# Kernel optimization log

Hardware: AMD Instinct MI355X
Metric: run time of the kernel (lower is better)

The kernel has to match this reference:

```python
import jax, jax.numpy as jnp
import numpy as np

B, T = 8, 5
C2, C1, C0 = 128, 256, 512  # in_channels = [C2, C1, C0]


def _ln(x, g, b):
    # LayerNorm over last (channel) axis
    m = jnp.mean(x, axis=-1, keepdims=True)
    v = jnp.var(x, axis=-1, keepdims=True)
    return (x - m) * jax.lax.rsqrt(v + 1e-5) * g + b


def _fuse_branch(x, gc, bc, gr, br, Wcur, Wref, bf, convw, bns, bnb):
    # x: [B, C, T, H, W]
    xt = jnp.transpose(x, (0, 2, 3, 4, 1))            # [B, T, H, W, C] (channel-last, like the permutes)
    cur = xt[:, -1]                                    # [B, H, W, C] last frame
    refs = xt[:, :-1]                                  # [B, T-1, H, W, C]
    # ShiftVSS stand-in: cross-frame fuse with residual (vectorized over T-1 frames)
    cur_proj = jnp.einsum('bhwc,cd->bhwd', _ln(cur, gc, bc), Wcur)        # [B,H,W,C]
    ref_proj = jnp.einsum('bthwc,cd->bthwd', _ln(refs, gr, br), Wref)     # [B,T-1,H,W,C]
    h = cur[:, None] + jax.nn.silu(cur_proj[:, None] + ref_proj + bf)     # [B,T-1,H,W,C]
    # BaseConv 1x1: pointwise conv + folded-BN + SiLU
    y = jax.nn.silu(jnp.einsum('bthwc,cd->bthwd', h, convw) * bns + bnb)  # [B,T-1,H,W,C]
    # fused temporal max + avg pooling (AdaptiveMax/AvgPool3d to T=1)
    pooled = jnp.max(y, axis=1) + jnp.mean(y, axis=1)                     # [B,H,W,C]
    return jnp.transpose(pooled, (0, 3, 1, 2))                            # [B,C,H,W]


def setup_inputs() -> dict:
    key = jax.random.key(0)
    ks = jax.random.split(key, 32)

    def n(k, shape, s=1.0):
        return jax.random.normal(k, shape, dtype=jnp.float32) * s

    d = {}
    d['x2'] = n(ks[0], (B, C2, T, 64, 64))
    d['x1'] = n(ks[1], (B, C1, T, 32, 32))
    d['x0'] = n(ks[2], (B, C0, T, 16, 16))  # unused by forward, kept for signature fidelity
    for i, (p, C) in enumerate([('2', C2), ('1', C1)]):
        o = 3 + i * 4
        d[f'g{p}c'] = jnp.ones((C,), jnp.float32)
        d[f'b{p}c'] = jnp.zeros((C,), jnp.float32)
        d[f'g{p}r'] = jnp.ones((C,), jnp.float32)
        d[f'b{p}r'] = jnp.zeros((C,), jnp.float32)
        d[f'W{p}cur'] = n(ks[o], (C, C), 0.02)
        d[f'W{p}ref'] = n(ks[o + 1], (C, C), 0.02)
        d[f'bias{p}'] = jnp.zeros((C,), jnp.float32)
        d[f'convw{p}'] = n(ks[o + 2], (C, C), 0.02)
        d[f'bns{p}'] = jnp.ones((C,), jnp.float32)
        d[f'bnb{p}'] = jnp.zeros((C,), jnp.float32)
    return d


def reference(x2, x1, x0,
              g2c, b2c, g2r, b2r, W2cur, W2ref, bias2, convw2, bns2, bnb2,
              g1c, b1c, g1r, b1r, W1cur, W1ref, bias1, convw1, bns1, bnb1):
    x2_out = _fuse_branch(x2, g2c, b2c, g2r, b2r, W2cur, W2ref, bias2, convw2, bns2, bnb2)
    x1_out = _fuse_branch(x1, g1c, b1c, g1r, b1r, W1cur, W1ref, bias1, convw1, bns1, bnb1)
    return (x2_out, x1_out)
```

## Files before the change

### kernel.cpp

```cpp
#include <hip/hip_runtime.h>
#include <stdint.h>

#define DI __device__ __forceinline__

typedef __attribute__((ext_vector_type(8))) short short8;
typedef __attribute__((ext_vector_type(4))) short short4v;
typedef __attribute__((ext_vector_type(4))) float f32x4;

DI float bf2f(unsigned short u){ union{unsigned int i; float f;} v; v.i = ((unsigned int)u)<<16; return v.f; }
DI unsigned short f2bf(float f){ union{float f; unsigned int i;} v; v.f=f; return (unsigned short)((v.i + 0x7fffu + ((v.i>>16)&1u))>>16); }
DI float siluf(float x){ return x/(1.f + __expf(-x)); }
DI f32x4 vzero(){ f32x4 z; z[0]=0.f;z[1]=0.f;z[2]=0.f;z[3]=0.f; return z; }
DI f32x4 vsplat(float x){ f32x4 z; z[0]=x;z[1]=x;z[2]=x;z[3]=x; return z; }

struct PrepArgs {
  const float* W[6];
  const float* g[6];
  unsigned short* Wt[6];
  int C[6];
};

__global__ __launch_bounds__(256) void prep_transpose(PrepArgs a){
  int m = blockIdx.z;
  int C = a.C[m];
  int nt = C >> 5;
  if ((int)blockIdx.x >= nt || (int)blockIdx.y >= nt) return;
  __shared__ float tile[32][33];
  int col = threadIdx.x & 31;
  int rr  = threadIdx.x >> 5;
  const float* W = a.W[m];
  const float* g = a.g[m];
  #pragma unroll
  for (int p=0;p<4;++p){
    int r = rr + p*8;
    int cK = blockIdx.x*32 + r;
    int dN = blockIdx.y*32 + col;
    float v = W[(size_t)cK*C + dN];
    if (g) v *= g[cK];
    tile[r][col] = v;
  }
  __syncthreads();
  unsigned short* Wt = a.Wt[m];
  #pragma unroll
  for (int p=0;p<4;++p){
    int r = rr + p*8;
    int dN = blockIdx.y*32 + r;
    int cK = blockIdx.x*32 + col;
    Wt[(size_t)dN*C + cK] = f2bf(tile[col][r]);
  }
}

struct ColArgs {
  const float* W[4]; const float* g[4]; const float* b[4]; const float* extra[4];
  float* ocs[4]; float* obs[4]; int C[4];
};

__global__ __launch_bounds__(256) void prep_colsum(ColArgs a){
  int j = blockIdx.y;
  int C = a.C[j];
  int d0 = blockIdx.x * 64;
  if (d0 >= C) return;
  int dl = threadIdx.x & 63;
  int g  = threadIdx.x >> 6;
  int d  = d0 + dl;
  const float* W = a.W[j]; const float* gv = a.g[j]; const float* bv = a.b[j];
  float cs = 0.f, bs = 0.f;
  for (int c = g; c < C; c += 4){
    float gc = gv[c], bc = bv[c];
    float w = W[(size_t)c*C + d];
    cs += gc*w;
    bs += bc*w;
  }
  __shared__ float rcs[4][64], rbs[4][64];
  rcs[g][dl] = cs; rbs[g][dl] = bs;
  __syncthreads();
  if (threadIdx.x < 64){
    float c0 = rcs[0][dl]+rcs[1][dl]+rcs[2][dl]+rcs[3][dl];
    float b0 = rbs[0][dl]+rbs[1][dl]+rbs[2][dl]+rbs[3][dl];
    if (a.extra[j]) b0 += a.extra[j][d];
    a.ocs[j][d] = c0;
    a.obs[j][d] = b0;
  }
}


template<int C>
DI short8 readFrag(const short* S, int rowBase, int ks, int lane){
  int row = rowBase + (lane & 15);
  int chunk = (ks*4 + ((lane>>4)&3)) ^ (lane & 7);
  return *(const short8*)((const char*)S + row*(2*C) + chunk*16);
}

template<int C>
DI void stageA_x(const float* __restrict__ xb, int strideC, short* As,
                 float* red, float* smean, float* srstd){
  int tid = threadIdx.x;
  int px = tid & 63, g = tid >> 6;
  float sum = 0.f, sq = 0.f;
  #pragma unroll
  for (int it=0; it<C/16; ++it){
    int cb = it*16 + g*4;
    float v0 = xb[(size_t)(cb+0)*strideC + px];
    float v1 = xb[(size_t)(cb+1)*strideC + px];
    float v2 = xb[(size_t)(cb+2)*strideC + px];
    float v3 = xb[(size_t)(cb+3)*strideC + px];
    sum += v0+v1+v2+v3;
    sq  += v0*v0+v1*v1+v2*v2+v3*v3;
    short4v pk;
    pk[0]=(short)f2bf(v0); pk[1]=(short)f2bf(v1); pk[2]=(short)f2bf(v2); pk[3]=(short)f2bf(v3);
    int chunk = cb >> 3;
    *(short4v*)((char*)As + px*(2*C) + ((chunk ^ (px&7))*16) + (cb&7)*2) = pk;
  }
  red[g*64 + px] = sum;
  red[256 + g*64 + px] = sq;
  __syncthreads();
  if (tid < 64){
    float s=0.f, q=0.f;
    #pragma unroll
    for (int gg=0; gg<4; ++gg){ s += red[gg*64+tid]; q += red[256+gg*64+tid]; }
    float m = s*(1.f/C);
    float var = fmaxf(q*(1.f/C) - m*m, 0.f);
    smean[tid] = m;
    srstd[tid] = rsqrtf(var + 1e-5f);
  }
  __syncthreads();
}

template<int C, int ROWS>
DI void stageCopy(const unsigned short* __restrict__ src, short* dst){
  int tid = threadIdx.x;
  constexpr int CH = C/8;
  constexpr int IT = (ROWS*CH)/256;
  #pragma unroll
  for (int it=0; it<IT; ++it){
    int i = tid + it*256;
    int row = i / CH, ch = i % CH;
    short8 v = *(const short8*)(src + (size_t)row*C + ch*8);
    *(short8*)((char*)dst + row*(2*C) + ((ch ^ (row&7))*16)) = v;
  }
}

template<int C>
DI void mfmaLoop(const short* As, const short* Bs, f32x4 acc[2][4], int lane, int wr, int wc){
  #pragma unroll
  for (int ks=0; ks<C/32; ++ks){
    short8 a0 = readFrag<C>(As, wr*32 +  0, ks, lane);
    short8 a1 = readFrag<C>(As, wr*32 + 16, ks, lane);
    short8 b0 = readFrag<C>(Bs, wc*64 +  0, ks, lane);
    short8 b1 = readFrag<C>(Bs, wc*64 + 16, ks, lane);
    short8 b2 = readFrag<C>(Bs, wc*64 + 32, ks, lane);
    short8 b3 = readFrag<C>(Bs, wc*64 + 48, ks, lane);
    acc[0][0] = __builtin_amdgcn_mfma_f32_16x16x32_bf16(a0,b0,acc[0][0],0,0,0);
    acc[0][1] = __builtin_amdgcn_mfma_f32_16x16x32_bf16(a0,b1,acc[0][1],0,0,0);
    acc[0][2] = __builtin_amdgcn_mfma_f32_16x16x32_bf16(a0,b2,acc[0][2],0,0,0);
    acc[0][3] = __builtin_amdgcn_mfma_f32_16x16x32_bf16(a0,b3,acc[0][3],0,0,0);
    acc[1][0] = __builtin_amdgcn_mfma_f32_16x16x32_bf16(a1,b0,acc[1][0],0,0,0);
    acc[1][1] = __builtin_amdgcn_mfma_f32_16x16x32_bf16(a1,b1,acc[1][1],0,0,0);
    acc[1][2] = __builtin_amdgcn_mfma_f32_16x16x32_bf16(a1,b2,acc[1][2],0,0,0);
    acc[1][3] = __builtin_amdgcn_mfma_f32_16x16x32_bf16(a1,b3,acc[1][3],0,0,0);
  }
}

template<int C>
__global__ __launch_bounds__(256) void k1_curproj(
    const float* __restrict__ x, const unsigned short* __restrict__ Wt,
    const float* __restrict__ colsum, const float* __restrict__ bias,
    unsigned short* __restrict__ Pout, unsigned short* __restrict__ curT,
    int Npix, int HW){
  constexpr int T = 5;
  __shared__ __align__(16) short As[64*C];
  __shared__ __align__(16) short Bs[128*C];
  __shared__ float red[512];
  __shared__ float smean[64], srstd[64];

  int n0 = blockIdx.y*128;
  int px0 = blockIdx.x*64;
  int b = px0 / HW, hw0 = px0 % HW;
  const float* xb = x + ((size_t)b*C*T + (T-1))*HW + hw0;

  stageCopy<C,128>(Wt + (size_t)n0*C, Bs);
  stageA_x<C>(xb, T*HW, As, red, smean, srstd);

  int tid = threadIdx.x, lane = tid&63, wid = tid>>6, wr = wid>>1, wc = wid&1, hi = lane>>4;
  f32x4 acc[2][4];
  #pragma unroll
  for (int i=0;i<2;++i)
    #pragma unroll
    for (int j=0;j<4;++j) acc[i][j] = vzero();
  mfmaLoop<C>(As, Bs, acc, lane, wr, wc);

  if (n0 == 0){
    constexpr int CH = C/8;
    #pragma unroll
    for (int it=0; it<(64*CH)/256; ++it){
      int i = tid + it*256;
      int row = i/CH, ch = i%CH;
      short8 v = *(const short8*)((const char*)As + row*(2*C) + ((ch ^ (row&7))*16));
      *(short8*)(curT + (size_t)(px0+row)*C + ch*8) = v;
    }
  }

  #pragma unroll
  for (int nf=0; nf<4; ++nf){
    int d = n0 + wc*64 + nf*16 + (lane&15);
    float cs = colsum[d], bi = bias[d];
    #pragma unroll
    for (int mf=0; mf<2; ++mf){
      #pragma unroll
      for (int r=0; r<4; ++r){
        int pl = wr*32 + mf*16 + hi*4 + r;
        float P = srstd[pl]*(acc[mf][nf][r] - smean[pl]*cs) + bi;
        Pout[(size_t)(px0+pl)*C + d] = f2bf(P);
      }
    }
  }
}

template<int C>
__global__ __launch_bounds__(256) void k2_refproj(
    const float* __restrict__ x, const unsigned short* __restrict__ Wt,
    const float* __restrict__ colsum, const float* __restrict__ biasRf,
    const unsigned short* __restrict__ Pcur, const unsigned short* __restrict__ curT,
    unsigned short* __restrict__ hout, int Npix, int HW){
  constexpr int T = 5;
  __shared__ __align__(16) short As[64*C];
  __shared__ __align__(16) short Bs[128*C];
  __shared__ float red[512];
  __shared__ float smean[64], srstd[64];

  int n0 = blockIdx.y*128;
  int px0 = blockIdx.x*64;
  int t = blockIdx.z;
  int b = px0 / HW, hw0 = px0 % HW;
  const float* xb = x + ((size_t)b*C*T + t)*HW + hw0;

  stageCopy<C,128>(Wt + (size_t)n0*C, Bs);
  stageA_x<C>(xb, T*HW, As, red, smean, srstd);

  int tid = threadIdx.x, lane = tid&63, wid = tid>>6, wr = wid>>1, wc = wid&1, hi = lane>>4;
  f32x4 acc[2][4];
  #pragma unroll
  for (int i=0;i<2;++i)
    #pragma unroll
    for (int j=0;j<4;++j) acc[i][j] = vzero();
  mfmaLoop<C>(As, Bs, acc, lane, wr, wc);

  #pragma unroll
  for (int nf=0; nf<4; ++nf){
    int d = n0 + wc*64 + nf*16 + (lane&15);
    float cs = colsum[d], bi = biasRf[d];
    #pragma unroll
    for (int mf=0; mf<2; ++mf){
      #pragma unroll
      for (int r=0; r<4; ++r){
        int pl = wr*32 + mf*16 + hi*4 + r;
        size_t idx = (size_t)(px0+pl)*C + d;
        float pre = srstd[pl]*(acc[mf][nf][r] - smean[pl]*cs) + bi + bf2f(Pcur[idx]);
        float h = bf2f(curT[idx]) + siluf(pre);
        hout[(size_t)t*Npix*C + idx] = f2bf(h);
      }
    }
  }
}

template<int C>
__global__ __launch_bounds__(256) void k3_conv(
    const unsigned short* __restrict__ h, const unsigned short* __restrict__ WtV,
    const float* __restrict__ bns, const float* __restrict__ bnb,
    float* __restrict__ out, int Npix, int HW){
  constexpr int PB = 133;
  constexpr int AsBytes = 64*C*2;
  constexpr int PoolBytes = 64*PB*4;
  constexpr int U = (AsBytes > PoolBytes) ? AsBytes : PoolBytes;
  __shared__ __align__(16) char uni[U];
  __shared__ __align__(16) short Bs[128*C];
  short* As = (short*)uni;
  float* pool = (float*)uni;

  int n0 = blockIdx.y*128;
  int px0 = blockIdx.x*64;
  int b = px0 / HW, hw0 = px0 % HW;
  int tid = threadIdx.x, lane = tid&63, wid = tid>>6, wr = wid>>1, wc = wid&1, hi = lane>>4;

  stageCopy<C,128>(WtV + (size_t)n0*C, Bs);

  f32x4 mx[2][4], sm[2][4];
  #pragma unroll
  for (int i=0;i<2;++i)
    #pragma unroll
    for (int j=0;j<4;++j){ mx[i][j] = vsplat(-3.0e38f); sm[i][j] = vzero(); }

  for (int t=0; t<4; ++t){
    __syncthreads();
    stageCopy<C,64>(h + ((size_t)t*Npix + px0)*C, As);
    __syncthreads();
    f32x4 acc[2][4];
    #pragma unroll
    for (int i=0;i<2;++i)
      #pragma unroll
      for (int j=0;j<4;++j) acc[i][j] = vzero();
    mfmaLoop<C>(As, Bs, acc, lane, wr, wc);
    #pragma unroll
    for (int nf=0; nf<4; ++nf){
      int d = n0 + wc*64 + nf*16 + (lane&15);
      float s_ = bns[d], b_ = bnb[d];
      #pragma unroll
      for (int mf=0; mf<2; ++mf){
        #pragma unroll
        for (int r=0; r<4; ++r){
          float y = siluf(acc[mf][nf][r]*s_ + b_);
          mx[mf][nf][r] = fmaxf(mx[mf][nf][r], y);
          sm[mf][nf][r] += y;
        }
      }
    }
  }

  __syncthreads();
  #pragma unroll
  for (int nf=0; nf<4; ++nf){
    int dl = wc*64 + nf*16 + (lane&15);
    #pragma unroll
    for (int mf=0; mf<2; ++mf){
      #pragma unroll
      for (int r=0; r<4; ++r){
        int pl = wr*32 + mf*16 + hi*4 + r;
        pool[pl*PB + dl] = mx[mf][nf][r] + 0.25f*sm[mf][nf][r];
      }
    }
  }
  __syncthreads();

  #pragma unroll
  for (int it=0; it<8; ++it){
    int i = tid + it*256;
    int dl = i >> 4;
    int pq = (i & 15) * 4;
    f32x4 vv;
    #pragma unroll
    for (int k=0;k<4;++k) vv[k] = pool[(pq+k)*PB + dl];
    *(f32x4*)(out + (size_t)(b*C + n0 + dl)*HW + hw0 + pq) = vv;
  }
}

extern "C" void kernel_launch(void* const* d_in, const int* in_sizes, int n_in,
                              void* d_out, int out_size, void* d_ws, size_t ws_size,
                              hipStream_t stream) {
  (void)in_sizes; (void)n_in; (void)out_size; (void)ws_size;
  const float* x2    = (const float*)d_in[0];
  const float* x1    = (const float*)d_in[1];
  const float* g2c   = (const float*)d_in[3];
  const float* b2c   = (const float*)d_in[4];
  const float* g2r   = (const float*)d_in[5];
  const float* b2r   = (const float*)d_in[6];
  const float* W2cur = (const float*)d_in[7];
  const float* W2ref = (const float*)d_in[8];
  const float* bias2 = (const float*)d_in[9];
  const float* convw2= (const float*)d_in[10];
  const float* bns2  = (const float*)d_in[11];
  const float* bnb2  = (const float*)d_in[12];
  const float* g1c   = (const float*)d_in[13];
  const float* b1c   = (const float*)d_in[14];
  const float* g1r   = (const float*)d_in[15];
  const float* b1r   = (const float*)d_in[16];
  const float* W1cur = (const float*)d_in[17];
  const float* W1ref = (const float*)d_in[18];
  const float* bias1 = (const float*)d_in[19];
  const float* convw1= (const float*)d_in[20];
  const float* bns1  = (const float*)d_in[21];
  const float* bnb1  = (const float*)d_in[22];

  const int C2 = 128, C1 = 256;
  const int NP2 = 8*64*64, NP1 = 8*32*32;
  const int HW2 = 4096, HW1 = 1024;

  char* ws = (char*)d_ws;
  size_t off = 0;
  auto alloc = [&](size_t bytes){ size_t o = off; off = (off + bytes + 255) & ~(size_t)255; return o; };
  size_t oWtC2 = alloc((size_t)C2*C2*2), oWtR2 = alloc((size_t)C2*C2*2), oWtV2 = alloc((size_t)C2*C2*2);
  size_t oWtC1 = alloc((size_t)C1*C1*2), oWtR1 = alloc((size_t)C1*C1*2), oWtV1 = alloc((size_t)C1*C1*2);
  size_t oColC2 = alloc(C2*4), oBiasC2 = alloc(C2*4), oColR2 = alloc(C2*4), oBiasR2 = alloc(C2*4);
  size_t oColC1 = alloc(C1*4), oBiasC1 = alloc(C1*4), oColR1 = alloc(C1*4), oBiasR1 = alloc(C1*4);
  size_t oP2  = alloc((size_t)NP2*C2*2);
  size_t oCT2 = alloc((size_t)NP2*C2*2);
  size_t oH2  = alloc((size_t)4*NP2*C2*2);
  size_t oP1  = alloc((size_t)NP1*C1*2);
  size_t oCT1 = alloc((size_t)NP1*C1*2);
  size_t oH1  = alloc((size_t)4*NP1*C1*2);

  unsigned short* WtC2 = (unsigned short*)(ws + oWtC2);
  unsigned short* WtR2 = (unsigned short*)(ws + oWtR2);
  unsigned short* WtV2 = (unsigned short*)(ws + oWtV2);
  unsigned short* WtC1 = (unsigned short*)(ws + oWtC1);
  unsigned short* WtR1 = (unsigned short*)(ws + oWtR1);
  unsigned short* WtV1 = (unsigned short*)(ws + oWtV1);
  float* ColC2 = (float*)(ws + oColC2); float* BiasC2 = (float*)(ws + oBiasC2);
  float* ColR2 = (float*)(ws + oColR2); float* BiasR2 = (float*)(ws + oBiasR2);
  float* ColC1 = (float*)(ws + oColC1); float* BiasC1 = (float*)(ws + oBiasC1);
  float* ColR1 = (float*)(ws + oColR1); float* BiasR1 = (float*)(ws + oBiasR1);
  unsigned short* P2  = (unsigned short*)(ws + oP2);
  unsigned short* CT2 = (unsigned short*)(ws + oCT2);
  unsigned short* H2  = (unsigned short*)(ws + oH2);
  unsigned short* P1  = (unsigned short*)(ws + oP1);
  unsigned short* CT1 = (unsigned short*)(ws + oCT1);
  unsigned short* H1  = (unsigned short*)(ws + oH1);

  PrepArgs pa;
  pa.W[0]=W2cur;  pa.g[0]=g2c;     pa.Wt[0]=WtC2; pa.C[0]=C2;
  pa.W[1]=W2ref;  pa.g[1]=g2r;     pa.Wt[1]=WtR2; pa.C[1]=C2;
  pa.W[2]=convw2; pa.g[2]=nullptr; pa.Wt[2]=WtV2; pa.C[2]=C2;
  pa.W[3]=W1cur;  pa.g[3]=g1c;     pa.Wt[3]=WtC1; pa.C[3]=C1;
  pa.W[4]=W1ref;  pa.g[4]=g1r;     pa.Wt[4]=WtR1; pa.C[4]=C1;
  pa.W[5]=convw1; pa.g[5]=nullptr; pa.Wt[5]=WtV1; pa.C[5]=C1;
  prep_transpose<<<dim3(8,8,6), 256, 0, stream>>>(pa);

  ColArgs ca;
  ca.W[0]=W2cur; ca.g[0]=g2c; ca.b[0]=b2c; ca.extra[0]=nullptr; ca.ocs[0]=ColC2; ca.obs[0]=BiasC2; ca.C[0]=C2;
  ca.W[1]=W2ref; ca.g[1]=g2r; ca.b[1]=b2r; ca.extra[1]=bias2;   ca.ocs[1]=ColR2; ca.obs[1]=BiasR2; ca.C[1]=C2;
  ca.W[2]=W1cur; ca.g[2]=g1c; ca.b[2]=b1c; ca.extra[2]=nullptr; ca.ocs[2]=ColC1; ca.obs[2]=BiasC1; ca.C[2]=C1;
  ca.W[3]=W1ref; ca.g[3]=g1r; ca.b[3]=b1r; ca.extra[3]=bias1;   ca.ocs[3]=ColR1; ca.obs[3]=BiasR1; ca.C[3]=C1;
  prep_colsum<<<dim3(4, 4), 256, 0, stream>>>(ca);

  float* out2 = (float*)d_out;
  float* out1 = out2 + (size_t)8*C2*HW2;

  k1_curproj<128><<<dim3(NP2/64, 1),    256, 0, stream>>>(x2, WtC2, ColC2, BiasC2, P2, CT2, NP2, HW2);
  k1_curproj<256><<<dim3(NP1/64, 2),    256, 0, stream>>>(x1, WtC1, ColC1, BiasC1, P1, CT1, NP1, HW1);
  k2_refproj<128><<<dim3(NP2/64, 1, 4), 256, 0, stream>>>(x2, WtR2, ColR2, BiasR2, P2, CT2, H2, NP2, HW2);
  k2_refproj<256><<<dim3(NP1/64, 2, 4), 256, 0, stream>>>(x1, WtR1, ColR1, BiasR1, P1, CT1, H1, NP1, HW1);
  k3_conv<128><<<dim3(NP2/64, 1),       256, 0, stream>>>(H2, WtV2, bns2, bnb2, out2, NP2, HW2);
  k3_conv<256><<<dim3(NP1/64, 2),       256, 0, stream>>>(H1, WtV1, bns1, bnb1, out1, NP1, HW1);
}
```

Measured before the change: 141.1 us.

## Vectorize LN input loads and store cur projections in fragment-native layout

stageA_x now reads x with 16-byte vector loads along the pixel axis and scatters bf16 values into LDS. The LayerNorm statistics are then computed from LDS in a second pass. k1 writes the current-frame projection and the current-frame values in an MFMA-fragment-ordered layout, so k2 can read them with coalesced 16-byte loads instead of scalar strided gathers. k2 stages its h output through LDS so it can write coalesced short8 rows. The cost is an extra barrier and scalar 2-byte LDS scatter stores. The stats are now taken from bf16-rounded values, which slightly changes numerics.

```diff
diff --git a/kernel.cpp b/kernel.cpp
--- a/kernel.cpp
+++ b/kernel.cpp
@@ -4,7 +4,6 @@
 #define DI __device__ __forceinline__
 
 typedef __attribute__((ext_vector_type(8))) short short8;
-typedef __attribute__((ext_vector_type(4))) short short4v;
 typedef __attribute__((ext_vector_type(4))) float f32x4;
 
 DI float bf2f(unsigned short u){ union{unsigned int i; float f;} v; v.i = ((unsigned int)u)<<16; return v.f; }
@@ -95,24 +94,33 @@
 DI void stageA_x(const float* __restrict__ xb, int strideC, short* As,
                  float* red, float* smean, float* srstd){
   int tid = threadIdx.x;
-  int px = tid & 63, g = tid >> 6;
-  float sum = 0.f, sq = 0.f;
-  #pragma unroll
-  for (int it=0; it<C/16; ++it){
-    int cb = it*16 + g*4;
-    float v0 = xb[(size_t)(cb+0)*strideC + px];
-    float v1 = xb[(size_t)(cb+1)*strideC + px];
-    float v2 = xb[(size_t)(cb+2)*strideC + px];
-    float v3 = xb[(size_t)(cb+3)*strideC + px];
-    sum += v0+v1+v2+v3;
-    sq  += v0*v0+v1*v1+v2*v2+v3*v3;
-    short4v pk;
-    pk[0]=(short)f2bf(v0); pk[1]=(short)f2bf(v1); pk[2]=(short)f2bf(v2); pk[3]=(short)f2bf(v3);
-    int chunk = cb >> 3;
-    *(short4v*)((char*)As + px*(2*C) + ((chunk ^ (px&7))*16) + (cb&7)*2) = pk;
-  }
-  red[g*64 + px] = sum;
-  red[256 + g*64 + px] = sq;
+  int lane = tid & 63, w = tid >> 6;
+  #pragma unroll
+  for (int i=0; i<C/16; ++i){
+    int ic = i >> 2, ip = i & 3;
+    int c  = w*(C/4) + ic*16 + (lane & 15);
+    int pq = ip*4 + (lane >> 4);
+    f32x4 v = *(const f32x4*)(xb + (size_t)c*strideC + pq*4);
+    #pragma unroll
+    for (int j=0;j<4;++j){
+      int px = pq*4 + j;
+      *(unsigned short*)((char*)As + px*(2*C) + (((c>>3) ^ (px&7))*16) + (c&7)*2) = f2bf(v[j]);
+    }
+  }
+  __syncthreads();
+  {
+    int px = tid & 63, g = tid >> 6;
+    constexpr int PER = (C/8)/4;
+    float s=0.f, q=0.f;
+    #pragma unroll
+    for (int k=0;k<PER;++k){
+      int ch = g*PER + k;
+      short8 v = *(const short8*)((const char*)As + px*(2*C) + ((ch ^ (px&7))*16));
+      #pragma unroll
+      for (int e=0;e<8;++e){ float f = bf2f((unsigned short)v[e]); s += f; q += f*f; }
+    }
+    red[g*64+px] = s; red[256+g*64+px] = q;
+  }
   __syncthreads();
   if (tid < 64){
     float s=0.f, q=0.f;
@@ -165,15 +173,17 @@
 __global__ __launch_bounds__(256) void k1_curproj(
     const float* __restrict__ x, const unsigned short* __restrict__ Wt,
     const float* __restrict__ colsum, const float* __restrict__ bias,
-    unsigned short* __restrict__ Pout, unsigned short* __restrict__ curT,
+    unsigned short* __restrict__ Pf, unsigned short* __restrict__ CTf,
     int Npix, int HW){
   constexpr int T = 5;
+  constexpr int NY = C/128;
   __shared__ __align__(16) short As[64*C];
   __shared__ __align__(16) short Bs[128*C];
   __shared__ float red[512];
   __shared__ float smean[64], srstd[64];
 
-  int n0 = blockIdx.y*128;
+  int ny = blockIdx.y;
+  int n0 = ny*128;
   int px0 = blockIdx.x*64;
   int b = px0 / HW, hw0 = px0 % HW;
   const float* xb = x + ((size_t)b*C*T + (T-1))*HW + hw0;
@@ -182,6 +192,11 @@
   stageA_x<C>(xb, T*HW, As, red, smean, srstd);
 
   int tid = threadIdx.x, lane = tid&63, wid = tid>>6, wr = wid>>1, wc = wid&1, hi = lane>>4;
+
+  float csv[4], biv[4];
+  #pragma unroll
+  for (int nf=0;nf<4;++nf){ int d = n0 + wc*64 + nf*16 + (lane&15); csv[nf]=colsum[d]; biv[nf]=bias[d]; }
+
   f32x4 acc[2][4];
   #pragma unroll
   for (int i=0;i<2;++i)
@@ -189,30 +204,22 @@
     for (int j=0;j<4;++j) acc[i][j] = vzero();
   mfmaLoop<C>(As, Bs, acc, lane, wr, wc);
 
-  if (n0 == 0){
-    constexpr int CH = C/8;
-    #pragma unroll
-    for (int it=0; it<(64*CH)/256; ++it){
-      int i = tid + it*256;
-      int row = i/CH, ch = i%CH;
-      short8 v = *(const short8*)((const char*)As + row*(2*C) + ((ch ^ (row&7))*16));
-      *(short8*)(curT + (size_t)(px0+row)*C + ch*8) = v;
-    }
-  }
-
-  #pragma unroll
-  for (int nf=0; nf<4; ++nf){
-    int d = n0 + wc*64 + nf*16 + (lane&15);
-    float cs = colsum[d], bi = bias[d];
-    #pragma unroll
-    for (int mf=0; mf<2; ++mf){
-      #pragma unroll
-      for (int r=0; r<4; ++r){
-        int pl = wr*32 + mf*16 + hi*4 + r;
-        float P = srstd[pl]*(acc[mf][nf][r] - smean[pl]*cs) + bi;
-        Pout[(size_t)(px0+pl)*C + d] = f2bf(P);
+  size_t fb = ((size_t)(px0>>6)*NY + ny)*4;
+  #pragma unroll
+  for (int k=0;k<4;++k){
+    short8 pv, cv;
+    int dg = n0 + wc*64 + k*16 + (lane&15);
+    #pragma unroll
+    for (int mf=0;mf<2;++mf)
+      #pragma unroll
+      for (int r=0;r<4;++r){
+        int pl = wr*32+mf*16+hi*4+r;
+        float P = srstd[pl]*(acc[mf][k][r] - smean[pl]*csv[k]) + biv[k];
+        pv[mf*4+r] = (short)f2bf(P);
+        cv[mf*4+r] = (short)*(const unsigned short*)((const char*)As + pl*(2*C) + (((dg>>3)^(pl&7))*16) + (dg&7)*2);
       }
-    }
+    *(short8*)(Pf  + ((fb+k)*256 + tid)*8) = pv;
+    *(short8*)(CTf + ((fb+k)*256 + tid)*8) = cv;
   }
 }
 
@@ -220,15 +227,17 @@
 __global__ __launch_bounds__(256) void k2_refproj(
     const float* __restrict__ x, const unsigned short* __restrict__ Wt,
     const float* __restrict__ colsum, const float* __restrict__ biasRf,
-    const unsigned short* __restrict__ Pcur, const unsigned short* __restrict__ curT,
+    const unsigned short* __restrict__ Pf, const unsigned short* __restrict__ CTf,
     unsigned short* __restrict__ hout, int Npix, int HW){
   constexpr int T = 5;
+  constexpr int NY = C/128;
   __shared__ __align__(16) short As[64*C];
   __shared__ __align__(16) short Bs[128*C];
   __shared__ float red[512];
   __shared__ float smean[64], srstd[64];
 
-  int n0 = blockIdx.y*128;
+  int ny = blockIdx.y;
+  int n0 = ny*128;
   int px0 = blockIdx.x*64;
   int t = blockIdx.z;
   int b = px0 / HW, hw0 = px0 % HW;
@@ -238,6 +247,11 @@
   stageA_x<C>(xb, T*HW, As, red, smean, srstd);
 
   int tid = threadIdx.x, lane = tid&63, wid = tid>>6, wr = wid>>1, wc = wid&1, hi = lane>>4;
+
+  float csv[4], biv[4];
+  #pragma unroll
+  for (int nf=0;nf<4;++nf){ int d = n0 + wc*64 + nf*16 + (lane&15); csv[nf]=colsum[d]; biv[nf]=biasRf[d]; }
+
   f32x4 acc[2][4];
   #pragma unroll
   for (int i=0;i<2;++i)
@@ -245,21 +259,35 @@
     for (int j=0;j<4;++j) acc[i][j] = vzero();
   mfmaLoop<C>(As, Bs, acc, lane, wr, wc);
 
-  #pragma unroll
-  for (int nf=0; nf<4; ++nf){
-    int d = n0 + wc*64 + nf*16 + (lane&15);
-    float cs = colsum[d], bi = biasRf[d];
-    #pragma unroll
-    for (int mf=0; mf<2; ++mf){
-      #pragma unroll
-      for (int r=0; r<4; ++r){
-        int pl = wr*32 + mf*16 + hi*4 + r;
-        size_t idx = (size_t)(px0+pl)*C + d;
-        float pre = srstd[pl]*(acc[mf][nf][r] - smean[pl]*cs) + bi + bf2f(Pcur[idx]);
-        float h = bf2f(curT[idx]) + siluf(pre);
-        hout[(size_t)t*Npix*C + idx] = f2bf(h);
+  size_t fb = ((size_t)(px0>>6)*NY + ny)*4;
+  short8 pv[4], cv[4];
+  #pragma unroll
+  for (int k=0;k<4;++k){
+    pv[k] = *(const short8*)(Pf  + ((fb+k)*256 + tid)*8);
+    cv[k] = *(const short8*)(CTf + ((fb+k)*256 + tid)*8);
+  }
+  __syncthreads();
+  short* h_lds = As;
+  #pragma unroll
+  for (int nf=0;nf<4;++nf){
+    int dl = wc*64 + nf*16 + (lane&15);
+    #pragma unroll
+    for (int mf=0;mf<2;++mf)
+      #pragma unroll
+      for (int r=0;r<4;++r){
+        int pl = wr*32+mf*16+hi*4+r;
+        float pre = srstd[pl]*(acc[mf][nf][r]-smean[pl]*csv[nf]) + biv[nf] + bf2f((unsigned short)pv[nf][mf*4+r]);
+        float h = bf2f((unsigned short)cv[nf][mf*4+r]) + siluf(pre);
+        *(unsigned short*)((char*)h_lds + pl*256 + (((dl>>3)^(pl&7))*16) + (dl&7)*2) = f2bf(h);
       }
-    }
+  }
+  __syncthreads();
+  #pragma unroll
+  for (int it=0; it<4; ++it){
+    int i = tid + it*256;
+    int row = i >> 4, ch = i & 15;
+    short8 v = *(const short8*)((const char*)h_lds + row*256 + ((ch ^ (row&7))*16));
+    *(short8*)(hout + ((size_t)t*Npix + px0 + row)*C + n0 + ch*8) = v;
   }
 }
 
```

New measurement: 142.4 us. No clear change (+0.9%).
